# Performance work log

Hardware: AMD Instinct MI355X
Metric: run time of the kernel (lower is better)

The kernel has to match this reference:

```python
import jax, jax.numpy as jnp
import numpy as np

B, N, C, H = 4, 1025, 768, 12
KEEP_RATIO = 0.25
BETA = 1.0


def setup_inputs() -> dict:
    key = jax.random.key(0)
    k1, k2, k3, k4, k5 = jax.random.split(key, 5)
    x = jax.random.normal(k1, (B, N, C), dtype=jnp.float32)
    ucb_count_score = jax.random.uniform(k2, (H, N), dtype=jnp.float32)
    W_qkv = jax.random.normal(k3, (C, 3 * C), dtype=jnp.float32) * 0.02
    W_proj = jax.random.normal(k4, (C, C), dtype=jnp.float32) * 0.02
    b_proj = jax.random.normal(k5, (C,), dtype=jnp.float32) * 0.02
    return {"x": x, "ucb_count_score": ucb_count_score, "W_qkv": W_qkv,
            "W_proj": W_proj, "b_proj": b_proj, "counter": 100, "ucb_enabled": 1}


def reference(x, ucb_count_score, W_qkv, W_proj, b_proj, counter, ucb_enabled):
    Bn, Nn, Cn = x.shape
    Dh = Cn // H
    scale = Dh ** -0.5
    # qkv projection (no bias, qkv_bias=False)
    qkv = (x @ W_qkv).reshape(Bn, Nn, 3, H, Dh)
    q = jnp.transpose(qkv[:, :, 0], (0, 2, 1, 3))  # [B,H,N,Dh]
    k = jnp.transpose(qkv[:, :, 1], (0, 2, 1, 3))
    v = jnp.transpose(qkv[:, :, 2], (0, 2, 1, 3))
    attn_probs = jax.nn.softmax(jnp.einsum('bhnd,bhmd->bhnm', q, k) * scale, axis=-1)

    if ucb_enabled and counter > 50:
        # UCB pruning path (exclude_cls=True, keep_ratio set)
        total_patches = Nn - 1
        k_sel = max(1, int(total_patches * KEEP_RATIO))
        patch_scores = attn_probs[:, :, :, 1:].mean(axis=2)  # [B,H,N-1]
        expl = BETA * jnp.sqrt(jnp.log(counter + 1.0) / (ucb_count_score[:, 1:] + 1e-6))  # [H,N-1]
        global_ucb = (patch_scores + expl[None]).mean(axis=1)  # [B,N-1]
        _, sel = jax.lax.top_k(global_ucb, k_sel)  # [B,k]
        tok = sel + 1  # shift for CLS
        # keep[b,j] = 1 if token j is CLS or selected in batch b
        keep = jnp.zeros((Bn, Nn), dtype=attn_probs.dtype)
        keep = keep.at[jnp.arange(Bn)[:, None], tok].set(1.0).at[:, 0].set(1.0)
        # mask[b,h,i,j] = keep[b,i] OR keep[b,j]
        mask = jnp.maximum(keep[:, None, :, None], keep[:, None, None, :])
        pruned = attn_probs * mask
        pruned = pruned / (pruned.sum(axis=-1, keepdims=True) + 1e-8)
        context = jnp.einsum('bhnm,bhmd->bhnd', pruned, v)
        cnt = jnp.zeros((Nn,), dtype=jnp.float32).at[tok.reshape(-1)].add(1.0) / Bn
        score_delta = jnp.broadcast_to(cnt[None, :], ucb_count_score.shape)
    else:
        context = jnp.einsum('bhnm,bhmd->bhnd', attn_probs, v)
        score_delta = None

    out = context.transpose(0, 2, 1, 3).reshape(Bn, Nn, Cn) @ W_proj + b_proj
    return out, score_delta
```

## Files before the change

kernel.cpp:

```cpp
#include <hip/hip_runtime.h>
#include <hip/hip_bf16.h>
#include <math.h>

#define Bb 4
#define Nn 1025
#define Cc 768
#define Hh 12
#define BH (Bb*Hh)
#define M_ROWS 4100
#define KSEL 256
#define JP 1152
#define IT_TILES 68
#define NIB32 33
#define NSW 9
#define MT16 264
#define KC24 24
#define JT16 72
#define JT32 36
#define STR4 292
#define NPART 396
#define NSCORE 1024
#define QSCALE 0.18033688011112042f
#define MBIAS -30000.0f
#define OSTR 136

#define CAST_X_BLK 1584
#define CAST_WQKV_BLK 864
#define CAST_WPROJ_BLK 288

typedef __attribute__((ext_vector_type(8))) short short8;
typedef __attribute__((ext_vector_type(4))) float floatx4;
typedef __attribute__((ext_vector_type(4))) unsigned uintx4;

static __device__ inline unsigned short f2bf(float v) {
    __hip_bfloat16 b = __float2bfloat16(v);
    return *reinterpret_cast<unsigned short*>(&b);
}
static __device__ inline float fexp2(float x) {
    return __builtin_amdgcn_exp2f(x);
}
static __device__ inline unsigned pkbf(float lo, float hi) {
    union { float f; unsigned u; } a, b;
    a.f = lo; b.f = hi;
    return (a.u >> 16) | (b.u & 0xffff0000u);
}

static __device__ inline void async16(const unsigned short* g, unsigned short* l) {
    __builtin_amdgcn_global_load_lds(
        (const __attribute__((address_space(1))) unsigned int*)g,
        (__attribute__((address_space(3))) unsigned int*)l, 16, 0, 0);
}

__global__ __launch_bounds__(256)
void cast_all(const float* __restrict__ x, const float* __restrict__ Wqkv,
              const float* __restrict__ Wproj,
              unsigned short* __restrict__ xA, unsigned short* __restrict__ WB,
              unsigned short* __restrict__ WpB)
{
    int blk = blockIdx.x;
    int tid = threadIdx.x;
    if (blk < CAST_X_BLK) {
        int s = blk * 256 + tid;
        int ml = s & 15, q = (s >> 4) & 3;
        int t2 = s >> 6;
        int mt = t2 % MT16, kc = t2 / MT16;
        int m = mt * 16 + ml, k = kc * 32 + q * 8;
        uint4 pk = {0u, 0u, 0u, 0u};
        if (m < M_ROWS) {
            float4 a = *(const float4*)&x[(size_t)m * 768 + k];
            float4 b2 = *(const float4*)&x[(size_t)m * 768 + k + 4];
            pk.x = (unsigned)f2bf(a.x)  | ((unsigned)f2bf(a.y)  << 16);
            pk.y = (unsigned)f2bf(a.z)  | ((unsigned)f2bf(a.w)  << 16);
            pk.z = (unsigned)f2bf(b2.x) | ((unsigned)f2bf(b2.y) << 16);
            pk.w = (unsigned)f2bf(b2.z) | ((unsigned)f2bf(b2.w) << 16);
        }
        *(uint4*)&xA[(size_t)s * 8] = pk;
        return;
    }
    const float* W;
    unsigned short* WO;
    int N, NT, s;
    if (blk < CAST_X_BLK + CAST_WQKV_BLK) {
        W = Wqkv; WO = WB; N = 2304; NT = 144;
        s = (blk - CAST_X_BLK) * 256 + tid;
    } else {
        W = Wproj; WO = WpB; N = 768; NT = 48;
        s = (blk - CAST_X_BLK - CAST_WQKV_BLK) * 256 + tid;
    }
    int nl = s & 15, q = (s >> 4) & 3;
    int t2 = s >> 6;
    int nt = t2 % NT, kc = t2 / NT;
    int n = nt * 16 + nl, k = kc * 32 + q * 8;
    unsigned hv[8];
#pragma unroll
    for (int e = 0; e < 8; ++e)
        hv[e] = f2bf(W[(size_t)(k + e) * N + n]);
    uint4 pk;
    pk.x = hv[0] | (hv[1] << 16);
    pk.y = hv[2] | (hv[3] << 16);
    pk.z = hv[4] | (hv[5] << 16);
    pk.w = hv[6] | (hv[7] << 16);
    *(uint4*)&WO[(size_t)s * 8] = pk;
}

template<int NT, int MODE>
__global__ __launch_bounds__(256, 3)
void gemm_mfma(const unsigned short* __restrict__ Af,
               const unsigned short* __restrict__ Bf,
               int Nt16,
               unsigned short* __restrict__ qB, unsigned short* __restrict__ kF,
               unsigned short* __restrict__ vF,
               float* __restrict__ outp, const float* __restrict__ bias)
{
    __shared__ __align__(16) unsigned short smemU[(MODE == 0) ? (128 * OSTR) : (4096 + NT * 1024)];
    unsigned short* ldsA = smemU;
    unsigned short* ldsB = smemU + 4096;
    const int tid = threadIdx.x;
    const int ln = tid & 63, w = tid >> 6;
    const int wm = w >> 1, wn = w & 1;
    const int mb = blockIdx.x, nb = blockIdx.y;

    floatx4 acc[4][NT];
#pragma unroll
    for (int mt = 0; mt < 4; ++mt)
#pragma unroll
        for (int nt = 0; nt < NT; ++nt)
            acc[mt][nt] = (floatx4){0.f, 0.f, 0.f, 0.f};

    for (int kc = 0; kc < KC24; ++kc) {
        const unsigned short* gA = Af + ((size_t)(kc * MT16 + mb * 8)) * 512;
        const unsigned short* gB = Bf + ((size_t)(kc * Nt16 + nb * (NT * 2))) * 512;
        async16(gA + (size_t)(w * 128 + ln) * 8,      &ldsA[w * 1024]);
        async16(gA + (size_t)(w * 128 + 64 + ln) * 8, &ldsA[w * 1024 + 512]);
        if (NT == 4) {
            async16(gB + (size_t)(w * 128 + ln) * 8,      &ldsB[w * 1024]);
            async16(gB + (size_t)(w * 128 + 64 + ln) * 8, &ldsB[w * 1024 + 512]);
        } else {
            async16(gB + (size_t)(w * 64 + ln) * 8, &ldsB[w * 512]);
        }
        __syncthreads();

        short8 Am[4], Bn[NT];
#pragma unroll
        for (int mt = 0; mt < 4; ++mt)
            Am[mt] = *(const short8*)&ldsA[((wm * 4 + mt) * 64 + ln) * 8];
#pragma unroll
        for (int nt = 0; nt < NT; ++nt)
            Bn[nt] = *(const short8*)&ldsB[((wn * NT + nt) * 64 + ln) * 8];
#pragma unroll
        for (int mt = 0; mt < 4; ++mt)
#pragma unroll
            for (int nt = 0; nt < NT; ++nt)
                acc[mt][nt] = __builtin_amdgcn_mfma_f32_16x16x32_bf16(
                    Am[mt], Bn[nt], acc[mt][nt], 0, 0, 0);
        __syncthreads();
    }

    const int q = ln >> 4, l15 = ln & 15;
    if (MODE == 1) {
#pragma unroll
        for (int nt = 0; nt < NT; ++nt) {
            int gn = nb * (NT * 32) + wn * (NT * 16) + nt * 16 + l15;
            float bv = bias[gn];
#pragma unroll
            for (int mt = 0; mt < 4; ++mt) {
                int gmb = mb * 128 + wm * 64 + mt * 16 + q * 4;
#pragma unroll
                for (int r = 0; r < 4; ++r) {
                    int gm = gmb + r;
                    if (gm < M_ROWS)
                        outp[(size_t)gm * 768 + gn] = acc[mt][nt][r] + bv;
                }
            }
        }
    } else {
        const int s = (nb >= 12) ? 2 : (nb >= 6 ? 1 : 0);
        const float scl = (s == 0) ? QSCALE : 1.f;
        unsigned short* ldsO = smemU;
#pragma unroll
        for (int mt = 0; mt < 4; ++mt)
#pragma unroll
            for (int nt = 0; nt < NT; ++nt)
#pragma unroll
                for (int r = 0; r < 4; ++r) {
                    int row = wm * 64 + mt * 16 + q * 4 + r;
                    int col = wn * 64 + nt * 16 + l15;
                    ldsO[row * OSTR + col] = f2bf(acc[mt][nt][r] * scl);
                }
        __syncthreads();

        const int gm0 = mb * 128;
        if (s < 2) {
            const int c = tid >> 4;
            const int gn = nb * 128 + c * 8;
            const int rr = gn - s * Cc;
            const int h = rr >> 6, d0 = rr & 63;
#pragma unroll
            for (int rt = 0; rt < 8; ++rt) {
                int row = rt * 16 + (tid & 15);
                int gm = gm0 + row;
                if (gm >= M_ROWS) continue;
                int b = gm / Nn;
                int n = gm - b * Nn;
                int bh = b * Hh + h;
                uint4 v = *(const uint4*)&ldsO[row * OSTR + c * 8];
                if (s == 0) {
                    int idx = (((bh * IT_TILES + (n >> 4)) * 2 + (d0 >> 5)) * 512)
                              + ((((d0 & 31) >> 3) * 16 + (n & 15)) * 8);
                    *(uint4*)&qB[idx] = v;
                } else {
                    size_t idx = ((((size_t)bh * JT16 + (n >> 4)) * 2 + (d0 >> 5)) * 64
                                  + ((d0 >> 3) & 3) * 16 + (n & 15)) * 8;
                    *(uint4*)&kF[idx] = v;
                }
            }
        } else {
            int b0 = gm0 / Nn;
#pragma unroll 2
            for (int bi = 0; bi < 2; ++bi) {
                int b = b0 + bi;
                if (b >= Bb) break;
                int n0 = gm0 - b * Nn;
                int nlo = n0 < 0 ? 0 : n0;
                int nhi = n0 + 127;
                if (nhi > Nn - 1) nhi = Nn - 1;
                int nmx = M_ROWS - b * Nn - 1;
                if (nhi > nmx) nhi = nmx;
                if (nhi < nlo) continue;
                int ngl = nlo >> 3;
                int ngc = (nhi >> 3) - ngl + 1;
                for (int task = tid; task < 128 * ngc; task += 256) {
                    int dd = task & 127, ngi = task >> 7;
                    int nbase = (ngl + ngi) * 8;
                    int gn = nb * 128 + dd;
                    int rr = gn - 2 * Cc;
                    int h = rr >> 6, d = rr & 63;
                    int bh = b * Hh + h;
                    size_t idx = ((((size_t)bh * JT32 + (nbase >> 5)) * 4 + (d >> 4)) * 64
                                  + ((nbase >> 3) & 3) * 16 + (d & 15)) * 8;
                    if (nbase >= nlo && nbase + 7 <= nhi) {
                        int rowb = nbase - n0;
                        unsigned short vv[8];
#pragma unroll
                        for (int e = 0; e < 8; ++e)
                            vv[e] = ldsO[(rowb + e) * OSTR + dd];
                        *(uint4*)&vF[idx] = *(const uint4*)vv;
                    } else {
                        for (int e = 0; e < 8; ++e) {
                            int n = nbase + e;
                            if (n < nlo || n > nhi) continue;
                            vF[idx + e] = ldsO[(n - n0) * OSTR + dd];
                        }
                    }
                }
            }
        }
    }
}

__global__ __launch_bounds__(256, 4)
void attn_colsum_mfma(const unsigned short* __restrict__ qB,
                      const unsigned short* __restrict__ kF,
                      float* __restrict__ colsum_part)
{
    __shared__ unsigned int expS8[32 * STR4];
    __shared__ float red16[16][32];
    __shared__ float linv[32];

    const int blk = blockIdx.x;
    const int x8 = blk & 7, g = blk >> 3;
    const int bh = x8 * 6 + (g % 6);
    const int ib = g / 6;
    const int tid = threadIdx.x;
    const int ws = tid >> 6;
    const int ln = tid & 63;
    const int i16 = ln & 15, q = ln >> 4;

    const unsigned short* kBase = kF + (size_t)bh * JT16 * 1024;

    short8 Qf[2][2];
#pragma unroll
    for (int it = 0; it < 2; ++it)
#pragma unroll
        for (int kc = 0; kc < 2; ++kc)
            Qf[it][kc] = *(const short8*)&qB[(((size_t)bh * IT_TILES + ib * 2 + it) * 2 + kc) * 512 + ln * 8];

    float lacc[2][2] = {{0.f, 0.f}, {0.f, 0.f}};

    short8 Kc[2][2], Kn[2][2];
#pragma unroll
    for (int jt = 0; jt < 2; ++jt)
#pragma unroll
        for (int kc = 0; kc < 2; ++kc)
            Kc[jt][kc] = *(const short8*)&kBase[(((ws * 2 + jt) * 2 + kc) * 64 + ln) * 8];

    for (int sw = 0; sw < NSW; ++sw) {
        if (sw + 1 < NSW) {
#pragma unroll
            for (int jt = 0; jt < 2; ++jt)
#pragma unroll
                for (int kc = 0; kc < 2; ++kc)
                    Kn[jt][kc] = *(const short8*)&kBase[((((sw + 1) * 8 + ws * 2 + jt) * 2 + kc) * 64 + ln) * 8];
        }

        floatx4 S[2][2];
#pragma unroll
        for (int it = 0; it < 2; ++it)
#pragma unroll
            for (int jt = 0; jt < 2; ++jt) {
                S[it][jt] = (floatx4){0.f, 0.f, 0.f, 0.f};
#pragma unroll
                for (int kc = 0; kc < 2; ++kc)
                    S[it][jt] = __builtin_amdgcn_mfma_f32_16x16x32_bf16(Kc[jt][kc], Qf[it][kc], S[it][jt], 0, 0, 0);
            }

        const int jbase0 = sw * 128 + ws * 32 + q * 4;
#pragma unroll
        for (int it = 0; it < 2; ++it) {
            const int irow = it * 16 + i16;
#pragma unroll
            for (int jt = 0; jt < 2; ++jt) {
                int jbase = jbase0 + jt * 16;
                float p[4];
                if (sw < NSW - 1) {
#pragma unroll
                    for (int r = 0; r < 4; ++r)
                        p[r] = fexp2(S[it][jt][r]);
                } else {
#pragma unroll
                    for (int r = 0; r < 4; ++r) {
                        float vld = (jbase + r < Nn) ? 1.f : 0.f;
                        p[r] = fexp2(S[it][jt][r]) * vld;
                    }
                }
                lacc[it][jt] += (p[0] + p[1]) + (p[2] + p[3]);
                unsigned u = (unsigned)__builtin_amdgcn_cvt_pk_fp8_f32(p[0], p[1], 0, false);
                u = (unsigned)__builtin_amdgcn_cvt_pk_fp8_f32(p[2], p[3], (int)u, true);
                expS8[irow * STR4 + (jbase >> 2)] = u;
            }
        }
#pragma unroll
        for (int jt = 0; jt < 2; ++jt)
#pragma unroll
            for (int kc = 0; kc < 2; ++kc)
                Kc[jt][kc] = Kn[jt][kc];
    }

    __syncthreads();
#pragma unroll
    for (int it = 0; it < 2; ++it)
        red16[ws * 4 + q][it * 16 + i16] = lacc[it][0] + lacc[it][1];
    __syncthreads();
    if (tid < 32) {
        float s = 0.f;
#pragma unroll
        for (int t = 0; t < 16; ++t) s += red16[t][tid];
        int gi = ib * 32 + tid;
        linv[tid] = (gi < Nn) ? 1.f / s : 0.f;
    }
    __syncthreads();

    float* prow = colsum_part + (size_t)(bh * NIB32 + ib) * JP;
    for (int grp = tid; grp < 288; grp += 256) {
        float a0 = 0.f, a1 = 0.f, a2 = 0.f, a3 = 0.f;
#pragma unroll 8
        for (int i = 0; i < 32; ++i) {
            unsigned v = expS8[i * STR4 + grp];
            float li = linv[i];
            a0 += __builtin_amdgcn_cvt_f32_fp8(v, 0) * li;
            a1 += __builtin_amdgcn_cvt_f32_fp8(v, 1) * li;
            a2 += __builtin_amdgcn_cvt_f32_fp8(v, 2) * li;
            a3 += __builtin_amdgcn_cvt_f32_fp8(v, 3) * li;
        }
        float4 o = {a0, a1, a2, a3};
        *(float4*)&prow[grp * 4] = o;
    }
}

__global__ __launch_bounds__(256)
void colsum_reduce(const float* __restrict__ colsum_part,
                   const float* __restrict__ ucb_score,
                   const int* __restrict__ counter_p,
                   float* __restrict__ scoreF)
{
    const int b = blockIdx.x, jc = blockIdx.y;
    const int tid = threadIdx.x;
    const int j32 = tid & 31, grp = tid >> 5;
    const int t = jc * 32 + j32 + 1;
    __shared__ float red[8][32];

    const float* pb = colsum_part + (size_t)b * NPART * JP + t;
    float a0 = 0.f, a1 = 0.f;
    int r = grp;
    for (; r + 8 < NPART; r += 16) {
        a0 += pb[(size_t)r * JP];
        a1 += pb[(size_t)(r + 8) * JP];
    }
    for (; r < NPART; r += 8) a0 += pb[(size_t)r * JP];
    red[grp][j32] = a0 + a1;
    __syncthreads();

    if (tid < 32) {
        float cs = 0.f;
#pragma unroll
        for (int g = 0; g < 8; ++g) cs += red[g][tid];
        int tt = jc * 32 + tid + 1;
        float lc = logf((float)(*counter_p) + 1.0f);
        float s = cs * (1.0f / (float)Nn);
#pragma unroll
        for (int h = 0; h < Hh; ++h)
            s += sqrtf(lc / (ucb_score[h * Nn + tt] + 1e-6f));
        s *= (1.0f / (float)Hh);
        scoreF[b * NSCORE + tt - 1] = s;
    }
}

__global__ __launch_bounds__(1024)
void ucb_topk(const float* __restrict__ scoreF,
              float* __restrict__ keepP, float* __restrict__ cnt_b)
{
    const int b = blockIdx.x;
    const int tid = threadIdx.x;
    const int w = tid >> 6, ln = tid & 63;
    __shared__ int hist[8192];
    __shared__ int wtot[16];
    __shared__ unsigned ckey[1024];
    __shared__ int cidx[1024];
    __shared__ int s_tb, s_rem, ccount;

    for (int tpos = tid; tpos < JP; tpos += 1024) {
        keepP[b * JP + tpos] = 0.f;
        cnt_b[b * JP + tpos] = 0.f;
    }

    const unsigned key = __float_as_uint(scoreF[b * NSCORE + tid]);

    for (int tpos = tid; tpos < 8192; tpos += 1024) hist[tpos] = 0;
    if (tid == 0) ccount = 0;
    __syncthreads();
    atomicAdd(&hist[key >> 18], 1);
    __syncthreads();

    int part = 0;
#pragma unroll
    for (int q2 = 0; q2 < 8; ++q2) part += hist[tid * 8 + q2];
    int v = part;
#pragma unroll
    for (int off = 1; off < 64; off <<= 1) {
        int tv = __shfl_down(v, off);
        if (ln + off < 64) v += tv;
    }
    if (ln == 0) wtot[w] = v;
    __syncthreads();
    int woff = 0;
    for (int w2 = w + 1; w2 < 16; ++w2) woff += wtot[w2];
    int cum_above = v + woff - part;
    for (int q2 = 7; q2 >= 0; --q2) {
        int c = hist[tid * 8 + q2];
        if (cum_above < KSEL && cum_above + c >= KSEL) {
            s_tb = tid * 8 + q2;
            s_rem = KSEL - cum_above;
        }
        cum_above += c;
    }
    __syncthreads();

    const int tb = s_tb, rem = s_rem;
    const int mybin = (int)(key >> 18);
    bool sel = mybin > tb;
    if (mybin == tb) {
        int p = atomicAdd(&ccount, 1);
        ckey[p] = key; cidx[p] = tid;
    }
    __syncthreads();
    if (mybin == tb) {
        int rr = 0;
        const int cc = ccount;
        for (int c = 0; c < cc; ++c) {
            unsigned kc2 = ckey[c]; int ic = cidx[c];
            if (kc2 > key || (kc2 == key && ic < tid)) ++rr;
        }
        sel = rr < rem;
    }
    if (sel) {
        int tok = tid + 1;
        keepP[b * JP + tok] = 1.f;
        cnt_b[b * JP + tok] = 1.0f / (float)Bb;
    }
    if (tid == 0) keepP[b * JP + 0] = 1.f;
}

__global__ __launch_bounds__(256, 2)
void attn_ctx_mfma(const unsigned short* __restrict__ qB,
                   const unsigned short* __restrict__ kF,
                   const unsigned short* __restrict__ vF,
                   const float* __restrict__ keepP, const float* __restrict__ cnt_b,
                   unsigned short* __restrict__ ctxA, float* __restrict__ out2)
{
    __shared__ float keeps[JP];
    __shared__ float red16s[4][64];
    __shared__ float redC[64][66];

    const int blk = blockIdx.x;
    const int x8 = blk & 7, g = blk >> 3;
    const int bh = x8 * 6 + (g % 6);
    const int ib = g / 6;
    const int b = bh / Hh, h = bh % Hh;
    const int tid = threadIdx.x;
    const int ws = tid >> 6;
    const int ln = tid & 63;
    const int i16 = ln & 15, q = ln >> 4;

    {
        int t = blk * 256 + tid;
        if (t < Hh * Nn) {
            int n = t % Nn;
            out2[t] = cnt_b[0 * JP + n] + cnt_b[1 * JP + n]
                    + cnt_b[2 * JP + n] + cnt_b[3 * JP + n];
        }
    }

    for (int t = tid; t < JP; t += 256) keeps[t] = keepP[b * JP + t];

    const unsigned short* kBase = kF + (size_t)bh * JT16 * 1024;
    const unsigned short* vBase = vF + (size_t)bh * JT32 * 2048;

    short8 Qf[4][2];
#pragma unroll
    for (int it = 0; it < 4; ++it)
#pragma unroll
        for (int kc = 0; kc < 2; ++kc)
            Qf[it][kc] = *(const short8*)&qB[(((size_t)bh * IT_TILES + ib * 4 + it) * 2 + kc) * 512 + ln * 8];

    __syncthreads();

    float keepi[4];
#pragma unroll
    for (int it = 0; it < 4; ++it)
        keepi[it] = keeps[(ib * 4 + it) * 16 + i16];

    floatx4 ctxacc[4][4];
#pragma unroll
    for (int it = 0; it < 4; ++it)
#pragma unroll
        for (int dt = 0; dt < 4; ++dt)
            ctxacc[it][dt] = (floatx4){0.f, 0.f, 0.f, 0.f};
    floatx4 ds4[4];
#pragma unroll
    for (int it = 0; it < 4; ++it) ds4[it] = (floatx4){0.f, 0.f, 0.f, 0.f};

    const short obf = (short)0x3F80;
    const short8 onesB = {obf, obf, obf, obf, obf, obf, obf, obf};

    short8 Kc[2][2], Kn[2][2];
    short8 Vc8[4], Vn8[4];
#pragma unroll
    for (int jt = 0; jt < 2; ++jt)
#pragma unroll
        for (int kc = 0; kc < 2; ++kc)
            Kc[jt][kc] = *(const short8*)&kBase[(((ws * 2 + jt) * 2 + kc) * 64 + ln) * 8];
#pragma unroll
    for (int dt = 0; dt < 4; ++dt)
        Vc8[dt] = *(const short8*)&vBase[(((size_t)ws * 4 + dt) * 64 + ln) * 8];

    for (int sw = 0; sw < NSW; ++sw) {
        if (sw + 1 < NSW) {
#pragma unroll
            for (int jt = 0; jt < 2; ++jt)
#pragma unroll
                for (int kc = 0; kc < 2; ++kc)
                    Kn[jt][kc] = *(const short8*)&kBase[((((sw + 1) * 8 + ws * 2 + jt) * 2 + kc) * 64 + ln) * 8];
#pragma unroll
            for (int dt = 0; dt < 4; ++dt)
                Vn8[dt] = *(const short8*)&vBase[((((size_t)(sw + 1) * 4 + ws) * 4 + dt) * 64 + ln) * 8];
        }

        float biasK[2][4], biasN[2][4];
#pragma unroll
        for (int jt = 0; jt < 2; ++jt)
#pragma unroll
            for (int r = 0; r < 4; ++r) {
                int jj = sw * 128 + ws * 32 + jt * 16 + q * 4 + r;
                biasK[jt][r] = (jj < Nn) ? 0.f : MBIAS;
                biasN[jt][r] = (keeps[jj] - 1.f) * 30000.f;
            }

#pragma unroll
        for (int it = 0; it < 4; ++it) {
            bool rk = keepi[it] > 0.5f;
            floatx4 S[2];
#pragma unroll
            for (int jt = 0; jt < 2; ++jt)
#pragma unroll
                for (int r = 0; r < 4; ++r)
                    S[jt][r] = rk ? biasK[jt][r] : biasN[jt][r];
#pragma unroll
            for (int jt = 0; jt < 2; ++jt)
#pragma unroll
                for (int kc = 0; kc < 2; ++kc)
                    S[jt] = __builtin_amdgcn_mfma_f32_16x16x32_bf16(Kc[jt][kc], Qf[it][kc], S[jt], 0, 0, 0);

            float p0[4], p1[4];
#pragma unroll
            for (int r = 0; r < 4; ++r) {
                p0[r] = fexp2(S[0][r]);
                p1[r] = fexp2(S[1][r]);
            }
            unsigned Au = pkbf(p0[0], p0[1]);
            unsigned Bu = pkbf(p0[2], p0[3]);
            unsigned Cu = pkbf(p1[0], p1[1]);
            unsigned Du = pkbf(p1[2], p1[3]);
            asm("v_permlane32_swap_b32 %0, %1" : "+v"(Au), "+v"(Cu));
            asm("v_permlane32_swap_b32 %0, %1" : "+v"(Bu), "+v"(Du));
            asm("v_permlane16_swap_b32 %0, %1" : "+v"(Au), "+v"(Cu));
            asm("v_permlane16_swap_b32 %0, %1" : "+v"(Bu), "+v"(Du));
            short8 Wf = __builtin_bit_cast(short8, (uintx4){Au, Bu, Cu, Du});
#pragma unroll
            for (int dt = 0; dt < 4; ++dt)
                ctxacc[it][dt] = __builtin_amdgcn_mfma_f32_16x16x32_bf16(
                    Wf, Vc8[dt], ctxacc[it][dt], 0, 0, 0);
            ds4[it] = __builtin_amdgcn_mfma_f32_16x16x32_bf16(
                Wf, onesB, ds4[it], 0, 0, 0);
        }

#pragma unroll
        for (int jt = 0; jt < 2; ++jt)
#pragma unroll
            for (int kc = 0; kc < 2; ++kc)
                Kc[jt][kc] = Kn[jt][kc];
#pragma unroll
        for (int dt = 0; dt < 4; ++dt)
            Vc8[dt] = Vn8[dt];
    }

    __syncthreads();
    if (i16 == 0) {
#pragma unroll
        for (int it = 0; it < 4; ++it)
#pragma unroll
            for (int r = 0; r < 4; ++r)
                red16s[ws][it * 16 + q * 4 + r] = ds4[it][r];
    }
    for (int w = 0; w < 4; ++w) {
        __syncthreads();
        if (ws == w) {
#pragma unroll
            for (int it = 0; it < 4; ++it)
#pragma unroll
                for (int dt = 0; dt < 4; ++dt)
#pragma unroll
                    for (int r = 0; r < 4; ++r) {
                        int i = it * 16 + q * 4 + r;
                        int d = dt * 16 + i16;
                        float v = ctxacc[it][dt][r];
                        redC[i][d] = (w == 0) ? v : (redC[i][d] + v);
                    }
        }
    }
    __syncthreads();
#pragma unroll
    for (int rep = 0; rep < 2; ++rep) {
        int s2 = tid + rep * 256;
        int i = s2 >> 3, dc = s2 & 7;
        int gi = ib * 64 + i;
        if (gi < Nn) {
            int m = b * Nn + gi;
            float den = red16s[0][i] + red16s[1][i] + red16s[2][i] + red16s[3][i];
            float dv = 1.f / (den + 1e-8f);
            const float* src = &redC[i][dc * 8];
            uint4 pk;
            pk.x = (unsigned)f2bf(src[0] * dv) | ((unsigned)f2bf(src[1] * dv) << 16);
            pk.y = (unsigned)f2bf(src[2] * dv) | ((unsigned)f2bf(src[3] * dv) << 16);
            pk.z = (unsigned)f2bf(src[4] * dv) | ((unsigned)f2bf(src[5] * dv) << 16);
            pk.w = (unsigned)f2bf(src[6] * dv) | ((unsigned)f2bf(src[7] * dv) << 16);
            int kc2 = h * 2 + (dc >> 2);
            int q2 = dc & 3;
            size_t idx = (((size_t)(kc2 * MT16 + (m >> 4))) * 64 + q2 * 16 + (m & 15)) * 8;
            *(uint4*)&ctxA[idx] = pk;
        }
    }
}

extern "C" void kernel_launch(void* const* d_in, const int* in_sizes, int n_in,
                              void* d_out, int out_size, void* d_ws, size_t ws_size,
                              hipStream_t stream) {
    const float* x     = (const float*)d_in[0];
    const float* ucb   = (const float*)d_in[1];
    const float* Wqkv  = (const float*)d_in[2];
    const float* Wproj = (const float*)d_in[3];
    const float* bproj = (const float*)d_in[4];
    const int*   counter = (const int*)d_in[5];

    unsigned short* qB = (unsigned short*)d_ws;
    unsigned short* kF = qB + 3342336;
    unsigned short* vF = kF + 3538944;
    float* keepP    = (float*)(vF + 3538944);
    float* cnt_b    = keepP + 4608;
    unsigned short* ctxA = (unsigned short*)(cnt_b + 4608);
    unsigned short* xA   = ctxA + 3244032;
    unsigned short* WB   = xA + 3244032;
    unsigned short* WpB  = WB + 1769472;
    float* colsum_part = (float*)(WpB + 589824);
    float* scoreF = colsum_part + 1824768;

    float* out  = (float*)d_out;
    float* out2 = out + 3148800;

    cast_all<<<dim3(CAST_X_BLK + CAST_WQKV_BLK + CAST_WPROJ_BLK), dim3(256), 0, stream>>>(
        x, Wqkv, Wproj, xA, WB, WpB);
    gemm_mfma<4, 0><<<dim3(33, 18), dim3(256), 0, stream>>>(
        xA, WB, 144, qB, kF, vF, nullptr, nullptr);
    attn_colsum_mfma<<<dim3(8 * 198), dim3(256), 0, stream>>>(qB, kF, colsum_part);
    colsum_reduce<<<dim3(Bb, 32), dim3(256), 0, stream>>>(colsum_part, ucb, counter, scoreF);
    ucb_topk<<<dim3(Bb), dim3(1024), 0, stream>>>(scoreF, keepP, cnt_b);
    attn_ctx_mfma<<<dim3(8 * 102), dim3(256), 0, stream>>>(qB, kF, vF, keepP, cnt_b, ctxA, out2);
    gemm_mfma<2, 1><<<dim3(33, 12), dim3(256), 0, stream>>>(
        ctxA, WpB, 48, nullptr, nullptr, nullptr, out, bproj);
}
```

Measured before the change: 193.1 us.

## Split context attention into kept-row full pass and pruned-row sparse pass via gathers

Exploits the pruning mask structure: kept query rows attend to all keys, while pruned rows only attend to the 257 kept keys. Top-k now emits a compacted list of kept indices. A new gather kernel packs Q rows, K and V for the kept tokens, and the context kernel runs two block types: full-length passes over the kept queries and 3-step passes over the gathered keys for the other queries. This removes the masked-out score and PV work, at the cost of an extra gather launch, extra workspace and more complex output indexing.

Measured after the change: 197.0 us. +2.0%, slower.

```diff
diff --git a/kernel.cpp b/kernel.cpp
--- a/kernel.cpp
+++ b/kernel.cpp
@@ -6,7 +6,6 @@
 #define Nn 1025
 #define Cc 768
 #define Hh 12
-#define BH (Bb*Hh)
 #define M_ROWS 4100
 #define KSEL 256
 #define JP 1152
@@ -20,6 +19,12 @@
 #define STR4 292
 #define NPART 396
 #define NSCORE 1024
+#define KT 17
+#define KVG 9
+#define QGT 20
+#define KGT 24
+#define KVG2 12
+#define KIS 320
 #define QSCALE 0.18033688011112042f
 #define MBIAS -30000.0f
 #define OSTR 136
@@ -417,13 +422,15 @@
 
 __global__ __launch_bounds__(1024)
 void ucb_topk(const float* __restrict__ scoreF,
-              float* __restrict__ keepP, float* __restrict__ cnt_b)
+              float* __restrict__ keepP, float* __restrict__ cnt_b,
+              int* __restrict__ keptIdx)
 {
     const int b = blockIdx.x;
     const int tid = threadIdx.x;
     const int w = tid >> 6, ln = tid & 63;
     __shared__ int hist[8192];
     __shared__ int wtot[16];
+    __shared__ int wcnt[16];
     __shared__ unsigned ckey[1024];
     __shared__ int cidx[1024];
     __shared__ int s_tb, s_rem, ccount;
@@ -432,6 +439,8 @@
         keepP[b * JP + tpos] = 0.f;
         cnt_b[b * JP + tpos] = 0.f;
     }
+    for (int tpos = tid; tpos < KIS; tpos += 1024)
+        keptIdx[b * KIS + tpos] = -1;
 
     const unsigned key = __float_as_uint(scoreF[b * NSCORE + tid]);
 
@@ -488,24 +497,81 @@
         cnt_b[b * JP + tok] = 1.0f / (float)Bb;
     }
     if (tid == 0) keepP[b * JP + 0] = 1.f;
+
+    unsigned long long m = __ballot(sel);
+    int rk = (int)__popcll(m & ((1ull << ln) - 1ull));
+    if (ln == 0) wcnt[w] = (int)__popcll(m);
+    __syncthreads();
+    int off2 = 1;
+    for (int w2 = 0; w2 < w; ++w2) off2 += wcnt[w2];
+    if (sel) keptIdx[b * KIS + off2 + rk] = tid + 1;
+    if (tid == 0) keptIdx[b * KIS + 0] = 0;
+}
+
+__global__ __launch_bounds__(256)
+void gather_kv(const unsigned short* __restrict__ qB, const unsigned short* __restrict__ kF,
+               const unsigned short* __restrict__ vF, const int* __restrict__ keptIdx,
+               unsigned short* __restrict__ qG, unsigned short* __restrict__ kG,
+               unsigned short* __restrict__ vG)
+{
+    const int blk = blockIdx.x, tid = threadIdx.x;
+    if (blk < 408) {
+        int sid = blk * 256 + tid;
+        int lane = sid & 63, kc = (sid >> 6) & 1;
+        int t = (sid >> 7) % KT, bh = (sid >> 7) / KT;
+        int np = t * 16 + (lane & 15), lh = lane >> 4, b = bh / Hh;
+        int src = keptIdx[b * KIS + np];
+        uint4 v = {0u, 0u, 0u, 0u};
+        if (src >= 0)
+            v = *(const uint4*)&qB[((((size_t)bh * IT_TILES + (src >> 4)) * 2 + kc) * 64
+                                    + lh * 16 + (src & 15)) * 8];
+        *(uint4*)&qG[((((size_t)bh * QGT + t) * 2 + kc) * 64 + lane) * 8] = v;
+    } else if (blk < 816) {
+        int sid = (blk - 408) * 256 + tid;
+        int lane = sid & 63, kc = (sid >> 6) & 1;
+        int t = (sid >> 7) % KT, bh = (sid >> 7) / KT;
+        int jp = t * 16 + (lane & 15), lh = lane >> 4, b = bh / Hh;
+        int src = keptIdx[b * KIS + jp];
+        uint4 v = {0u, 0u, 0u, 0u};
+        if (src >= 0)
+            v = *(const uint4*)&kF[((((size_t)bh * JT16 + (src >> 4)) * 2 + kc) * 64
+                                    + lh * 16 + (src & 15)) * 8];
+        *(uint4*)&kG[((((size_t)bh * KGT + t) * 2 + kc) * 64 + lane) * 8] = v;
+    } else {
+        int sid = (blk - 816) * 256 + tid;
+        int lane = sid & 63, dt = (sid >> 6) & 3;
+        int g = (sid >> 8) % KVG, bh = (sid >> 8) / KVG, b = bh / Hh;
+        unsigned short vv[8];
+#pragma unroll
+        for (int e = 0; e < 8; ++e) {
+            int jp = g * 32 + (lane >> 4) * 8 + e;
+            int src = keptIdx[b * KIS + jp];
+            vv[e] = 0;
+            if (src >= 0)
+                vv[e] = vF[((((size_t)bh * JT32 + (src >> 5)) * 4 + dt) * 64
+                            + ((src >> 3) & 3) * 16 + (lane & 15)) * 8 + (src & 7)];
+        }
+        *(uint4*)&vG[((((size_t)bh * KVG2 + g) * 4 + dt) * 64 + lane) * 8] =
+            *(uint4*)vv;
+    }
 }
 
 __global__ __launch_bounds__(256, 2)
-void attn_ctx_mfma(const unsigned short* __restrict__ qB,
-                   const unsigned short* __restrict__ kF,
-                   const unsigned short* __restrict__ vF,
-                   const float* __restrict__ keepP, const float* __restrict__ cnt_b,
-                   unsigned short* __restrict__ ctxA, float* __restrict__ out2)
+void attn_ctx_split(const unsigned short* __restrict__ qB,
+                    const unsigned short* __restrict__ qG,
+                    const unsigned short* __restrict__ kF,
+                    const unsigned short* __restrict__ kG,
+                    const unsigned short* __restrict__ vF,
+                    const unsigned short* __restrict__ vG,
+                    const float* __restrict__ keepP, const float* __restrict__ cnt_b,
+                    const int* __restrict__ keptIdx,
+                    unsigned short* __restrict__ ctxA, float* __restrict__ out2)
 {
-    __shared__ float keeps[JP];
     __shared__ float red16s[4][64];
     __shared__ float redC[64][66];
 
     const int blk = blockIdx.x;
-    const int x8 = blk & 7, g = blk >> 3;
-    const int bh = x8 * 6 + (g % 6);
-    const int ib = g / 6;
-    const int b = bh / Hh, h = bh % Hh;
+    const int x8 = blk & 7, g0 = blk >> 3;
     const int tid = threadIdx.x;
     const int ws = tid >> 6;
     const int ln = tid & 63;
@@ -520,24 +586,33 @@
         }
     }
 
-    for (int t = tid; t < JP; t += 256) keeps[t] = keepP[b * JP + t];
-
-    const unsigned short* kBase = kF + (size_t)bh * JT16 * 1024;
-    const unsigned short* vBase = vF + (size_t)bh * JT32 * 2048;
+    const bool isK2 = (g0 < 30);
+    int bh, rblk, nsw, jlim;
+    const unsigned short *qSrc0, *kSrc, *vSrc;
+    if (isK2) {
+        bh = x8 * 6 + (g0 % 6);
+        rblk = g0 / 6;
+        nsw = NSW; jlim = Nn;
+        qSrc0 = qG + ((size_t)bh * QGT + rblk * 4) * 1024;
+        kSrc = kF + (size_t)bh * JT16 * 1024;
+        vSrc = vF + (size_t)bh * JT32 * 2048;
+    } else {
+        int gg = g0 - 30;
+        bh = x8 * 6 + (gg % 6);
+        rblk = gg / 6;
+        nsw = 3; jlim = 257;
+        qSrc0 = qB + ((size_t)bh * IT_TILES + rblk * 4) * 1024;
+        kSrc = kG + (size_t)bh * KGT * 1024;
+        vSrc = vG + (size_t)bh * KVG2 * 2048;
+    }
+    const int b = bh / Hh, h = bh % Hh;
 
     short8 Qf[4][2];
 #pragma unroll
     for (int it = 0; it < 4; ++it)
 #pragma unroll
         for (int kc = 0; kc < 2; ++kc)
-            Qf[it][kc] = *(const short8*)&qB[(((size_t)bh * IT_TILES + ib * 4 + it) * 2 + kc) * 512 + ln * 8];
-
-    __syncthreads();
-
-    float keepi[4];
-#pragma unroll
-    for (int it = 0; it < 4; ++it)
-        keepi[it] = keeps[(ib * 4 + it) * 16 + i16];
+            Qf[it][kc] = *(const short8*)&qSrc0[(size_t)(it * 2 + kc) * 512 + ln * 8];
 
     floatx4 ctxacc[4][4];
 #pragma unroll
@@ -558,42 +633,40 @@
     for (int jt = 0; jt < 2; ++jt)
 #pragma unroll
         for (int kc = 0; kc < 2; ++kc)
-            Kc[jt][kc] = *(const short8*)&kBase[(((ws * 2 + jt) * 2 + kc) * 64 + ln) * 8];
+            Kc[jt][kc] = *(const short8*)&kSrc[(size_t)((ws * 2 + jt) * 2 + kc) * 512 + ln * 8];
 #pragma unroll
     for (int dt = 0; dt < 4; ++dt)
-        Vc8[dt] = *(const short8*)&vBase[(((size_t)ws * 4 + dt) * 64 + ln) * 8];
-
-    for (int sw = 0; sw < NSW; ++sw) {
-        if (sw + 1 < NSW) {
+        Vc8[dt] = *(const short8*)&vSrc[(size_t)(ws * 4 + dt) * 512 + ln * 8];
+
+    for (int sw = 0; sw < nsw; ++sw) {
+        if (sw + 1 < nsw) {
 #pragma unroll
             for (int jt = 0; jt < 2; ++jt)
 #pragma unroll
                 for (int kc = 0; kc < 2; ++kc)
-                    Kn[jt][kc] = *(const short8*)&kBase[((((sw + 1) * 8 + ws * 2 + jt) * 2 + kc) * 64 + ln) * 8];
+                    Kn[jt][kc] = *(const short8*)&kSrc[(size_t)(((sw + 1) * 8 + ws * 2 + jt) * 2 + kc) * 512 + ln * 8];
 #pragma unroll
             for (int dt = 0; dt < 4; ++dt)
-                Vn8[dt] = *(const short8*)&vBase[((((size_t)(sw + 1) * 4 + ws) * 4 + dt) * 64 + ln) * 8];
-        }
-
-        float biasK[2][4], biasN[2][4];
+                Vn8[dt] = *(const short8*)&vSrc[(size_t)(((sw + 1) * 4 + ws) * 4 + dt) * 512 + ln * 8];
+        }
+
+        float biasv[2][4];
 #pragma unroll
         for (int jt = 0; jt < 2; ++jt)
 #pragma unroll
             for (int r = 0; r < 4; ++r) {
                 int jj = sw * 128 + ws * 32 + jt * 16 + q * 4 + r;
-                biasK[jt][r] = (jj < Nn) ? 0.f : MBIAS;
-                biasN[jt][r] = (keeps[jj] - 1.f) * 30000.f;
+                biasv[jt][r] = (jj < jlim) ? 0.f : MBIAS;
             }
 
 #pragma unroll
         for (int it = 0; it < 4; ++it) {
-            bool rk = keepi[it] > 0.5f;
             floatx4 S[2];
 #pragma unroll
             for (int jt = 0; jt < 2; ++jt)
 #pragma unroll
                 for (int r = 0; r < 4; ++r)
-                    S[jt][r] = rk ? biasK[jt][r] : biasN[jt][r];
+                    S[jt][r] = biasv[jt][r];
 #pragma unroll
             for (int jt = 0; jt < 2; ++jt)
 #pragma unroll
@@ -662,17 +735,23 @@
     for (int rep = 0; rep < 2; ++rep) {
         int s2 = tid + rep * 256;
         int i = s2 >> 3, dc = s2 & 7;
-        int gi = ib * 64 + i;
-        if (gi < Nn) {
-            int m = b * Nn + gi;
+        int m = -1;
+        if (isK2) {
+            int src = keptIdx[b * KIS + rblk * 64 + i];
+            if (src >= 0) m = b * Nn + src;
+        } else {
+            int gi = rblk * 64 + i;
+            if (gi < Nn && keepP[b * JP + gi] < 0.5f) m = b * Nn + gi;
+        }
+        if (m >= 0) {
             float den = red16s[0][i] + red16s[1][i] + red16s[2][i] + red16s[3][i];
             float dv = 1.f / (den + 1e-8f);
-            const float* src = &redC[i][dc * 8];
+            const float* src8 = &redC[i][dc * 8];
             uint4 pk;
-            pk.x = (unsigned)f2bf(src[0] * dv) | ((unsigned)f2bf(src[1] * dv) << 16);
-            pk.y = (unsigned)f2bf(src[2] * dv) | ((unsigned)f2bf(src[3] * dv) << 16);
-            pk.z = (unsigned)f2bf(src[4] * dv) | ((unsigned)f2bf(src[5] * dv) << 16);
-            pk.w = (unsigned)f2bf(src[6] * dv) | ((unsigned)f2bf(src[7] * dv) << 16);
+            pk.x = (unsigned)f2bf(src8[0] * dv) | ((unsigned)f2bf(src8[1] * dv) << 16);
+            pk.y = (unsigned)f2bf(src8[2] * dv) | ((unsigned)f2bf(src8[3] * dv) << 16);
+            pk.z = (unsigned)f2bf(src8[4] * dv) | ((unsigned)f2bf(src8[5] * dv) << 16);
+            pk.w = (unsigned)f2bf(src8[6] * dv) | ((unsigned)f2bf(src8[7] * dv) << 16);
             int kc2 = h * 2 + (dc >> 2);
             int q2 = dc & 3;
             size_t idx = (((size_t)(kc2 * MT16 + (m >> 4))) * 64 + q2 * 16 + (m & 15)) * 8;
@@ -702,6 +781,10 @@
     unsigned short* WpB  = WB + 1769472;
     float* colsum_part = (float*)(WpB + 589824);
     float* scoreF = colsum_part + 1824768;
+    int* keptIdx  = (int*)(scoreF + 4096);
+    unsigned short* qG = (unsigned short*)(keptIdx + 4 * KIS);
+    unsigned short* kG = qG + 983040;
+    unsigned short* vG = kG + 1179648;
 
     float* out  = (float*)d_out;
     float* out2 = out + 3148800;
@@ -712,8 +795,10 @@
         xA, WB, 144, qB, kF, vF, nullptr, nullptr);
     attn_colsum_mfma<<<dim3(8 * 198), dim3(256), 0, stream>>>(qB, kF, colsum_part);
     colsum_reduce<<<dim3(Bb, 32), dim3(256), 0, stream>>>(colsum_part, ucb, counter, scoreF);
-    ucb_topk<<<dim3(Bb), dim3(1024), 0, stream>>>(scoreF, keepP, cnt_b);
-    attn_ctx_mfma<<<dim3(8 * 102), dim3(256), 0, stream>>>(qB, kF, vF, keepP, cnt_b, ctxA, out2);
+    ucb_topk<<<dim3(Bb), dim3(1024), 0, stream>>>(scoreF, keepP, cnt_b, keptIdx);
+    gather_kv<<<dim3(1248), dim3(256), 0, stream>>>(qB, kF, vF, keptIdx, qG, kG, vG);
+    attn_ctx_split<<<dim3(8 * 132), dim3(256), 0, stream>>>(
+        qB, qG, kF, kG, vF, vG, keepP, cnt_b, keptIdx, ctxA, out2);
     gemm_mfma<2, 1><<<dim3(33, 12), dim3(256), 0, stream>>>(
         ctxA, WpB, 48, nullptr, nullptr, nullptr, out, bproj);
 }
```
